# Kernel tuning notes

Hardware: AMD Instinct MI355X
Metric: run time of the kernel (lower is better)

The kernel has to match this reference:

```python
import jax, jax.numpy as jnp
import numpy as np

B, S, H = 4096, 15, 1024
PQ, CFG = 1003, 128
IN = PQ + 5 + 10 + 3 + 3  # 1024, matches input_size in torch module
EPS = 1e-5


def lstm_cell(x, h, c, Wih, Whh, bih, bhh):
    # PyTorch LSTMCell gate order: i, f, g, o
    gates = x @ Wih.T + bih + h @ Whh.T + bhh
    i, f, g, o = jnp.split(gates, 4, axis=-1)
    c2 = jax.nn.sigmoid(f) * c + jax.nn.sigmoid(i) * jnp.tanh(g)
    h2 = jax.nn.sigmoid(o) * jnp.tanh(c2)
    return h2, c2


def setup_inputs() -> dict:
    key = jax.random.key(0)
    ks = jax.random.split(key, 16)
    g = lambda i, shape, s=0.02: jax.random.normal(ks[i], shape, jnp.float32) * s
    u = lambda i, shape: jax.random.uniform(ks[i], shape, jnp.float32, -1.0, 1.0)
    return {
        "input_p_q": jax.random.normal(ks[0], (B, S, PQ), jnp.float32),
        "input_config": jax.random.normal(ks[1], (B, S, CFG), jnp.float32),
        "input_time": jax.random.randint(ks[2], (B, S, 3), 0, 5),
        "W_cfg": g(3, (10, CFG)), "b_cfg": jnp.zeros((10,), jnp.float32),
        "emb_hour": g(4, (24, 5), 1.0),
        "emb_weekday": g(5, (8, 3), 1.0),
        "emb_season": g(6, (5, 3), 1.0),
        # init(): uniform(-1,1) weights, zero bias for the two attention layers
        "W_sa": u(7, (IN, IN + 2 * H)), "b_sa": jnp.zeros((IN,), jnp.float32),
        "Wih_s": g(8, (4 * H, IN)), "Whh_s": g(9, (4 * H, H)),
        "bih_s": jnp.zeros((4 * H,), jnp.float32), "bhh_s": jnp.zeros((4 * H,), jnp.float32),
        "Wih_t": g(10, (4 * H, H)), "Whh_t": g(11, (4 * H, H)),
        "bih_t": jnp.zeros((4 * H,), jnp.float32), "bhh_t": jnp.zeros((4 * H,), jnp.float32),
        "W_ta": u(12, (1, 3 * H)), "b_ta": jnp.zeros((1,), jnp.float32),
        "bn_gamma": jnp.ones((S,), jnp.float32), "bn_beta": jnp.zeros((S,), jnp.float32),
        "Wih_d": g(13, (4, H)), "Whh_d": g(14, (4, 1)),
        "bih_d": jnp.zeros((4,), jnp.float32), "bhh_d": jnp.zeros((4,), jnp.float32),
    }


def reference(input_p_q, input_config, input_time,
              W_cfg, b_cfg, emb_hour, emb_weekday, emb_season,
              W_sa, b_sa, Wih_s, Whh_s, bih_s, bhh_s,
              Wih_t, Whh_t, bih_t, bhh_t, W_ta, b_ta,
              bn_gamma, bn_beta, Wih_d, Whh_d, bih_d, bhh_d):
    cfg = input_config @ W_cfg.T + b_cfg                       # [B,S,10]
    hr = emb_hour[input_time[:, :, 0]]                         # [B,S,5]
    wd = emb_weekday[input_time[:, :, 1]]                      # [B,S,3]
    sn = emb_season[input_time[:, :, 2]]                       # [B,S,3]
    inputs = jnp.concatenate([input_p_q, cfg, hr, wd, sn], axis=2)  # [B,S,IN]

    Bsz, Ssz = inputs.shape[0], inputs.shape[1]
    Hd = Whh_s.shape[1]
    h0 = jnp.zeros((Bsz, Hd), inputs.dtype)

    # ---- spatial encoder with per-step attention gating ----
    def step1(carry, x):
        h, c = carry
        score = jnp.tanh(jnp.concatenate([h, c, x], axis=1) @ W_sa.T + b_sa)
        h2, c2 = lstm_cell(x * score, h, c, Wih_s, Whh_s, bih_s, bhh_s)
        return (h2, c2), h2

    _, mid = jax.lax.scan(step1, (h0, h0), jnp.swapaxes(inputs, 0, 1))  # [S,B,H]
    mid = jnp.swapaxes(mid, 0, 1)                                      # [B,S,H]

    # ---- BatchNorm1d(15) in training mode: channels = sequence dim ----
    mu = mid.mean(axis=(0, 2), keepdims=True)
    var = mid.var(axis=(0, 2), keepdims=True)  # biased variance, as torch uses for normalization
    mid = (mid - mu) * jax.lax.rsqrt(var + EPS) * bn_gamma[None, :, None] + bn_beta[None, :, None]

    # ---- temporal encoder with post-step attention score ----
    def step2(carry, x):
        h, c = carry
        h2, c2 = lstm_cell(x, h, c, Wih_t, Whh_t, bih_t, bhh_t)
        att = jnp.tanh(jnp.concatenate([h2, c2, x], axis=1) @ W_ta.T + b_ta)  # [B,1]
        return (h2, c2), (h2, att)

    _, (outs, att2) = jax.lax.scan(step2, (h0, h0), jnp.swapaxes(mid, 0, 1))
    outs = jnp.swapaxes(outs, 0, 1)   # [B,S,H]
    att2 = jnp.swapaxes(att2, 0, 1)   # [B,S,1]

    # ---- decoder nn.LSTM (batch_first=False!) scans over the BATCH axis ----
    hd0 = jnp.zeros((Ssz, 1), outs.dtype)

    def step3(carry, x):
        h, c = carry
        h2, c2 = lstm_cell(x, h, c, Wih_d, Whh_d, bih_d, bhh_d)
        return (h2, c2), h2

    _, out1d = jax.lax.scan(step3, (hd0, hd0), outs)  # [B,S,1]

    sm = jax.nn.softmax(att2, axis=1)  # [B,S,1]
    # bmm(out1d^T [B,1,S], sm [B,S,1]) -> [B,1,1]
    out = jnp.einsum('bs,bs->b', out1d[:, :, 0], sm[:, :, 0])[:, None, None]
    return out
```

## Files before the change

kernel.cpp:

```cpp
#include <hip/hip_runtime.h>

#define AS1 __attribute__((address_space(1)))
#define AS3 __attribute__((address_space(3)))

typedef __attribute__((ext_vector_type(8))) _Float16 f16x8;
typedef __attribute__((ext_vector_type(4))) float f32x4;

static constexpr int BATCH = 4096;
static constexpr int SEQ   = 15;

__device__ __forceinline__ float h2f(unsigned short u) {
  return (float)__builtin_bit_cast(_Float16, u);
}
__device__ __forceinline__ unsigned short f2h(float f) {
  return __builtin_bit_cast(unsigned short, (_Float16)f);
}
__device__ __forceinline__ float frcp(float x) { return __builtin_amdgcn_rcpf(x); }
__device__ __forceinline__ float sigm(float x)  { return frcp(1.0f + __expf(-x)); }
__device__ __forceinline__ float tanhx(float x) { return 1.0f - 2.0f * frcp(1.0f + __expf(2.0f * x)); }

template<int STAGE>
__global__ __launch_bounds__(512, 2)
void gemm_lstm256(const unsigned short* A0, int lda0, int K0,
                  const unsigned short* A1, int lda1,
                  const unsigned short* Bw, int K,
                  const float* ib, float* Cst,
                  unsigned short* P0, unsigned short* P1, unsigned short* P2,
                  float* F0)
{
  __shared__ unsigned short lds[2][2][16384];
  const int tid  = threadIdx.x;
  const int wid  = tid >> 6;
  const int lane = tid & 63;
  const int wr = wid >> 2;
  const int wc = wid & 3;
  const int NT = K >> 6;

  const int bid = blockIdx.y * gridDim.x + blockIdx.x;
  const int cpx = (gridDim.x * gridDim.y) >> 3;
  const int swz = (bid & 7) * cpx + (bid >> 3);
  const int row0 = (swz / gridDim.x) * 256;
  const int col0 = (swz % gridDim.x) * 256;

  auto stage_half = [&](int bb, int mat, int hh, int kt) {
    const int k0 = kt * 64;
    const unsigned short* Ap; int lda, kc, rb;
    if (mat == 0) {
      if (k0 < K0) { Ap = A0; lda = lda0; kc = k0; }
      else         { Ap = A1; lda = lda1; kc = k0 - K0; }
      rb = row0;
    } else { Ap = Bw; lda = K; kc = k0; rb = col0; }
#pragma unroll
    for (int i = 0; i < 2; ++i) {
      const int x  = (tid + i * 512) * 16;
      const int xs = x ^ (((x >> 9) & 1) << 5);
      const int r  = hh * 128 + (xs >> 7);
      const int cb = xs & 127;
      const unsigned short* src = Ap + (size_t)(rb + r) * lda + kc + (cb >> 1);
      __builtin_amdgcn_global_load_lds((const AS1 void*)src,
          (AS3 void*)((char*)&lds[bb][mat][0] + hh * 16384 + wid * 1024 + i * 8192),
          16, 0, 0);
    }
  };

  const int frow = lane & 15;
  const int axor = ((lane >> 2) & 1) << 5;
  const int abase = ((((wr * 128 + frow) << 7) + (((lane >> 4) & 3) << 4))) ^ axor;
  const int bbase = ((((wc * 64  + frow) << 7) + (((lane >> 4) & 3) << 4))) ^ axor;

  const f32x4 zero = {0.f, 0.f, 0.f, 0.f};
  f32x4 acc[8][4];
#pragma unroll
  for (int i = 0; i < 8; ++i)
#pragma unroll
    for (int j = 0; j < 4; ++j) acc[i][j] = zero;

  stage_half(0, 0, 0, 0);
  stage_half(0, 0, 1, 0);
  stage_half(0, 1, 0, 0);
  stage_half(0, 1, 1, 0);
  if (NT > 1) { stage_half(1, 1, 0, 1); stage_half(1, 1, 1, 1); }
  asm volatile("s_waitcnt vmcnt(4)" ::: "memory");
  __builtin_amdgcn_s_barrier();

#define DO_PHASE(MB, STG, VMW)                                                        \
  {                                                                                   \
    const f16x8 a0 = *(const f16x8*)(ldsA + abase + (MB)     * 2048);                 \
    const f16x8 a1 = *(const f16x8*)(ldsA + abase + (MB)     * 2048 + 64);            \
    const f16x8 a2 = *(const f16x8*)(ldsA + abase + (MB + 1) * 2048);                 \
    const f16x8 a3 = *(const f16x8*)(ldsA + abase + (MB + 1) * 2048 + 64);            \
    STG;                                                                              \
    __builtin_amdgcn_s_barrier();                                                     \
    asm volatile("s_waitcnt lgkmcnt(0)" ::: "memory");                                \
    __builtin_amdgcn_sched_barrier(0);                                                \
    __builtin_amdgcn_s_setprio(1);                                                    \
    _Pragma("unroll")                                                                 \
    for (int n = 0; n < 4; ++n) {                                                     \
      acc[MB][n]     = __builtin_amdgcn_mfma_f32_16x16x32_f16(a0, bv[n][0], acc[MB][n],     0, 0, 0); \
      acc[MB][n]     = __builtin_amdgcn_mfma_f32_16x16x32_f16(a1, bv[n][1], acc[MB][n],     0, 0, 0); \
      acc[MB + 1][n] = __builtin_amdgcn_mfma_f32_16x16x32_f16(a2, bv[n][0], acc[MB + 1][n], 0, 0, 0); \
      acc[MB + 1][n] = __builtin_amdgcn_mfma_f32_16x16x32_f16(a3, bv[n][1], acc[MB + 1][n], 0, 0, 0); \
    }                                                                                 \
    __builtin_amdgcn_s_setprio(0);                                                    \
    VMW;                                                                              \
    __builtin_amdgcn_s_barrier();                                                     \
  }

  for (int kt = 0; kt < NT; ++kt) {
    const int cur = kt & 1;
    const char* ldsA = (const char*)&lds[cur][0][0];
    const char* ldsB = (const char*)&lds[cur][1][0];
    f16x8 bv[4][2];
#pragma unroll
    for (int n = 0; n < 4; ++n) {
      bv[n][0] = *(const f16x8*)(ldsB + bbase + n * 2048);
      bv[n][1] = *(const f16x8*)(ldsB + bbase + n * 2048 + 64);
    }
    DO_PHASE(0, { if (kt + 1 < NT) stage_half(cur ^ 1, 0, 0, kt + 1); }, { (void)0; });
    DO_PHASE(2, { if (kt + 1 < NT) stage_half(cur ^ 1, 0, 1, kt + 1); }, { (void)0; });
    DO_PHASE(4, { if (kt + 2 < NT) stage_half(cur,     1, 0, kt + 2); }, { (void)0; });
    DO_PHASE(6, { if (kt + 2 < NT) stage_half(cur,     1, 1, kt + 2); },
             { if (kt >= NT - 2) { asm volatile("s_waitcnt vmcnt(0)" ::: "memory"); }
               else              { asm volatile("s_waitcnt vmcnt(4)" ::: "memory"); } });
  }
#undef DO_PHASE

  float* xw = ((float*)&lds[0][0][0]) + wid * 256;
  const int cs = lane & 3;
  const int er = (lane >> 4) << 2;
  const int uq = (lane >> 2) & 3;

  float cold[8][4];
#pragma unroll
  for (int mi = 0; mi < 8; ++mi)
#pragma unroll
    for (int ni = 0; ni < 4; ++ni) {
      const int R = row0 + wr * 128 + mi * 16 + er + cs;
      const int U = ((col0 + wc * 64 + ni * 16) >> 2) + uq;
      cold[mi][ni] = Cst[(size_t)R * 1024 + U];
    }

#pragma unroll
  for (int mi = 0; mi < 8; ++mi)
#pragma unroll
    for (int ni = 0; ni < 4; ++ni) {
      __builtin_amdgcn_wave_barrier();
      *(f32x4*)(xw + lane * 4) = acc[mi][ni];
      __builtin_amdgcn_wave_barrier();
      __builtin_amdgcn_sched_barrier(0);
      const int qb = (lane & 60) * 4;
      const float g0 = xw[qb + 0  + cs];
      const float g1 = xw[qb + 4  + cs];
      const float g2 = xw[qb + 8  + cs];
      const float g3 = xw[qb + 12 + cs];
      __builtin_amdgcn_wave_barrier();
      const int R = row0 + wr * 128 + mi * 16 + er + cs;
      const int U = ((col0 + wc * 64 + ni * 16) >> 2) + uq;
      const f32x4 b4 = *(const f32x4*)(ib + 4 * U);
      const float gi = g0 + b4[0];
      const float gf = g1 + b4[1];
      const float gg = g2 + b4[2];
      const float go = g3 + b4[3];
      const size_t off = (size_t)R * 1024 + U;
      const float cn = sigm(gf) * cold[mi][ni] + sigm(gi) * tanhx(gg);
      const float hn = sigm(go) * tanhx(cn);
      Cst[off] = cn;
      const unsigned short hb = f2h(hn);
      if (STAGE == 1) {
        P0[(size_t)R * 2048 + U]        = hb;
        P0[(size_t)R * 2048 + 1024 + U] = f2h(cn);
        P1[(size_t)R * 2048 + 1024 + U] = hb;
        P2[off] = hb;
      } else {
        F0[off] = hn;
        P0[off] = hb;
      }
    }
}

template<int BM, int BN, int NWM, int NWN>
__global__ __launch_bounds__(256)
void gemm_score(const unsigned short* A0, int lda0, int K0,
                const unsigned short* A1, int lda1,
                const unsigned short* Bw,
                const float* bias, const unsigned short* X,
                unsigned short* OutG, int ldo, int N, int K)
{
  static_assert(NWM * NWN == 4, "4 waves");
  constexpr int FM = BM / (NWM * 16);
  constexpr int FN = BN / (NWN * 16);
  __shared__ unsigned short As[BM * 64];
  __shared__ unsigned short Bs[BN * 64];
  const int tid  = threadIdx.x;
  const int wid  = tid >> 6;
  const int lane = tid & 63;
  const int bid = blockIdx.y * gridDim.x + blockIdx.x;
  const int cpx = (gridDim.x * gridDim.y) >> 3;
  const int swz = (bid & 7) * cpx + (bid >> 3);
  const int row0 = (swz / gridDim.x) * BM;
  const int col0 = (swz % gridDim.x) * BN;
  const int wr = wid / NWN;
  const int wc = wid % NWN;
  const int l8 = lane >> 3;
  const int l7 = (lane & 7) * 8;
  const int frow = lane & 15;
  const int fcol = (lane >> 4) * 8;

  const f32x4 zero = {0.f, 0.f, 0.f, 0.f};
  f32x4 acc[FM][FN];
#pragma unroll
  for (int i = 0; i < FM; ++i)
#pragma unroll
    for (int j = 0; j < FN; ++j) acc[i][j] = zero;

  for (int k0 = 0; k0 < K; k0 += 64) {
    __syncthreads();
    const unsigned short* Ap; int lda, kc;
    if (k0 < K0) { Ap = A0; lda = lda0; kc = k0; }
    else         { Ap = A1; lda = lda1; kc = k0 - K0; }
#pragma unroll
    for (int ch = 0; ch < BM / 32; ++ch) {
      const int c = ch * 4 + wid;
      const unsigned short* src = Ap + (size_t)(row0 + c * 8 + l8) * lda + kc + l7;
      __builtin_amdgcn_global_load_lds((const AS1 void*)src, (AS3 void*)(As + c * 512), 16, 0, 0);
    }
#pragma unroll
    for (int ch = 0; ch < BN / 32; ++ch) {
      const int c = ch * 4 + wid;
      const unsigned short* src = Bw + (size_t)(col0 + c * 8 + l8) * K + k0 + l7;
      __builtin_amdgcn_global_load_lds((const AS1 void*)src, (AS3 void*)(Bs + c * 512), 16, 0, 0);
    }
    __syncthreads();
#pragma unroll
    for (int kk = 0; kk < 2; ++kk) {
      f16x8 av[FM], bv[FN];
#pragma unroll
      for (int mi = 0; mi < FM; ++mi)
        av[mi] = *(const f16x8*)(As + (wr * FM * 16 + mi * 16 + frow) * 64 + kk * 32 + fcol);
#pragma unroll
      for (int ni = 0; ni < FN; ++ni)
        bv[ni] = *(const f16x8*)(Bs + (wc * FN * 16 + ni * 16 + frow) * 64 + kk * 32 + fcol);
#pragma unroll
      for (int mi = 0; mi < FM; ++mi)
#pragma unroll
        for (int ni = 0; ni < FN; ++ni)
          acc[mi][ni] = __builtin_amdgcn_mfma_f32_16x16x32_f16(av[mi], bv[ni], acc[mi][ni], 0, 0, 0);
    }
  }

  const int erow = (lane >> 4) * 4;
#pragma unroll
  for (int mi = 0; mi < FM; ++mi)
#pragma unroll
    for (int ni = 0; ni < FN; ++ni) {
      const int row = row0 + wr * FM * 16 + mi * 16 + erow;
      const int col = col0 + wc * FN * 16 + ni * 16 + frow;
      const float bs = bias[col];
#pragma unroll
      for (int r = 0; r < 4; ++r) {
        const float v = tanhx(acc[mi][ni][r] + bs);
        const float xv = h2f(X[(size_t)(row + r) * N + col]);
        OutG[(size_t)(row + r) * ldo + col] = f2h(xv * v);
      }
    }
}

__global__ void f2h_copy(const float* src, unsigned short* dst, int n) {
  const int i = blockIdx.x * 256 + threadIdx.x;
  if (i < n) dst[i] = f2h(src[i]);
}

__global__ void cat_w_int(const float* wih, const float* whh, unsigned short* dst) {
  const int i = blockIdx.x * 256 + threadIdx.x;
  const int n = i >> 11, k = i & 2047;
  const int u = n >> 2, g = n & 3;
  const int src = g * 1024 + u;
  dst[i] = f2h(k < 1024 ? wih[src * 1024 + k] : whh[src * 1024 + (k - 1024)]);
}

__global__ void prep_bias(const float* bih, const float* bhh, float* ib) {
  const int i = blockIdx.x * 256 + threadIdx.x;
  const int u = i >> 2, g = i & 3;
  ib[i] = bih[g * 1024 + u] + bhh[g * 1024 + u];
}

__global__ void copy_pq(const float* pq, unsigned short* inb) {
  const int i4 = blockIdx.x * 256 + threadIdx.x;
  const float4 v = ((const float4*)pq)[i4];
  const int base = i4 * 4;
  const float vv[4] = {v.x, v.y, v.z, v.w};
#pragma unroll
  for (int e = 0; e < 4; ++e) {
    const int idx = base + e;
    const int bt = idx / 1003;
    const int j = idx - bt * 1003;
    const int b = bt / 15;
    const int t = bt - b * 15;
    inb[((size_t)t * BATCH + b) * 1024 + j] = f2h(vv[e]);
  }
}

__global__ void cfg_emb(const float* cfg, const int* tim,
                        const float* Wc, const float* bc,
                        const float* eh, const float* ew, const float* es,
                        unsigned short* inb)
{
  const int wv = (blockIdx.x * 256 + threadIdx.x) >> 6;
  const int lane = threadIdx.x & 63;
  const int b = wv / 15, t = wv - b * 15;
  const float* cp = cfg + (size_t)wv * 128;
  const float c0 = cp[lane], c1v = cp[lane + 64];
  unsigned short* dst = inb + ((size_t)t * BATCH + b) * 1024;
#pragma unroll
  for (int g = 0; g < 10; ++g) {
    float v = fmaf(c0, Wc[g * 128 + lane], c1v * Wc[g * 128 + 64 + lane]);
    v += __shfl_xor(v, 32); v += __shfl_xor(v, 16); v += __shfl_xor(v, 8);
    v += __shfl_xor(v, 4);  v += __shfl_xor(v, 2);  v += __shfl_xor(v, 1);
    if (lane == 0) dst[1003 + g] = f2h(v + bc[g]);
  }
  if (lane < 5)       dst[1013 + lane] = f2h(eh[tim[wv * 3 + 0] * 5 + lane]);
  else if (lane < 8)  dst[1018 + (lane - 5)] = f2h(ew[tim[wv * 3 + 1] * 3 + (lane - 5)]);
  else if (lane < 11) dst[1021 + (lane - 8)] = f2h(es[tim[wv * 3 + 2] * 3 + (lane - 8)]);
}

__global__ void bn_partial(const unsigned short* mid, float* part) {
  const int t = blockIdx.y, blk = blockIdx.x, tid = threadIdx.x;
  const unsigned short* p = mid + (size_t)t * BATCH * 1024;
  float s = 0.f, ss = 0.f;
  for (int i = blk * 256 + tid; i < BATCH * 1024; i += 128 * 256) {
    const float v = h2f(p[i]);
    s += v; ss += v * v;
  }
  for (int o = 32; o > 0; o >>= 1) { s += __shfl_down(s, o); ss += __shfl_down(ss, o); }
  __shared__ float sm[8];
  if ((tid & 63) == 0) { sm[(tid >> 6) * 2] = s; sm[(tid >> 6) * 2 + 1] = ss; }
  __syncthreads();
  if (tid == 0) {
    part[(t * 128 + blk) * 2]     = sm[0] + sm[2] + sm[4] + sm[6];
    part[(t * 128 + blk) * 2 + 1] = sm[1] + sm[3] + sm[5] + sm[7];
  }
}

__global__ void bn_final(const float* part, const float* gamma, const float* beta, float* scsh) {
  const int t = blockIdx.x, tid = threadIdx.x;
  float s = part[(t * 128 + tid) * 2], ss = part[(t * 128 + tid) * 2 + 1];
  for (int o = 32; o > 0; o >>= 1) { s += __shfl_down(s, o); ss += __shfl_down(ss, o); }
  __shared__ float sm[4];
  if ((tid & 63) == 0) { sm[(tid >> 6) * 2] = s; sm[(tid >> 6) * 2 + 1] = ss; }
  __syncthreads();
  if (tid == 0) {
    const float S = sm[0] + sm[2], SS = sm[1] + sm[3];
    const float inv = 1.f / (float)(BATCH * 1024);
    const float mu = S * inv;
    const float var = SS * inv - mu * mu;
    const float rstd = rsqrtf(var + 1e-5f);
    const float sc = rstd * gamma[t];
    scsh[t * 2] = sc;
    scsh[t * 2 + 1] = beta[t] - mu * sc;
  }
}

__global__ void bn_apply(unsigned short* mid, const float* scsh) {
  const int t = blockIdx.y;
  const int i = blockIdx.x * 256 + threadIdx.x;
  unsigned short* p = mid + (size_t)t * BATCH * 1024;
  p[i] = f2h(h2f(p[i]) * scsh[t * 2] + scsh[t * 2 + 1]);
}

__global__ void att_proj(const float* h2, const float* c2, const unsigned short* xn,
                         const float* Wta, const float* bta, const float* Wihd,
                         float* att2, float* proj, int t)
{
  const int b = blockIdx.x, tid = threadIdx.x;
  const float* h = h2 + (size_t)b * 1024;
  const float* c = c2 + (size_t)b * 1024;
  const unsigned short* x = xn + (size_t)b * 1024;
  float a = 0.f, p0 = 0.f, p1 = 0.f, p2 = 0.f, p3 = 0.f;
  for (int j = tid; j < 1024; j += 256) {
    const float hv = h[j], cv = c[j], xv = h2f(x[j]);
    a  += hv * Wta[j] + cv * Wta[1024 + j] + xv * Wta[2048 + j];
    p0 += hv * Wihd[j];
    p1 += hv * Wihd[1024 + j];
    p2 += hv * Wihd[2048 + j];
    p3 += hv * Wihd[3072 + j];
  }
  for (int o = 32; o > 0; o >>= 1) {
    a  += __shfl_down(a, o);  p0 += __shfl_down(p0, o); p1 += __shfl_down(p1, o);
    p2 += __shfl_down(p2, o); p3 += __shfl_down(p3, o);
  }
  __shared__ float sm[4][5];
  if ((tid & 63) == 0) {
    const int w = tid >> 6;
    sm[w][0] = a; sm[w][1] = p0; sm[w][2] = p1; sm[w][3] = p2; sm[w][4] = p3;
  }
  __syncthreads();
  if (tid == 0) {
    att2[b * SEQ + t] = tanhx(sm[0][0] + sm[1][0] + sm[2][0] + sm[3][0] + bta[0]);
    float* pp = proj + ((size_t)b * SEQ + t) * 4;
    pp[0] = sm[0][1] + sm[1][1] + sm[2][1] + sm[3][1];
    pp[1] = sm[0][2] + sm[1][2] + sm[2][2] + sm[3][2];
    pp[2] = sm[0][3] + sm[1][3] + sm[2][3] + sm[3][3];
    pp[3] = sm[0][4] + sm[1][4] + sm[2][4] + sm[3][4];
  }
}

__global__ __launch_bounds__(256) void lstm3_par(
    const float* proj, const float* Whhd,
    const float* bihd, const float* bhhd, float* out1d)
{
  const int s = blockIdx.x;
  const int tid = threadIdx.x;
  constexpr int CH = BATCH / 256;
  const float wi = Whhd[0], wf = Whhd[1], wg = Whhd[2], wo = Whhd[3];
  const float bi = bihd[0] + bhhd[0], bf_ = bihd[1] + bhhd[1];
  const float bg = bihd[2] + bhhd[2], bo = bihd[3] + bhhd[3];
  const float4* p4 = (const float4*)proj;
  float4 p[CH];
#pragma unroll
  for (int u = 0; u < CH; ++u) p[u] = p4[(tid * CH + u) * SEQ + s];
  __shared__ float Hb[257], Cb[257];
  Hb[tid] = 0.f; Cb[tid] = 0.f;
  if (tid == 255) { Hb[256] = 0.f; Cb[256] = 0.f; }
  __syncthreads();
  float h, c;
  for (int it = 0; it < 8; ++it) {
    h = Hb[tid]; c = Cb[tid];
#pragma unroll
    for (int u = 0; u < CH; ++u) {
      const float gi = fmaf(h, wi, p[u].x + bi);
      const float gf = fmaf(h, wf, p[u].y + bf_);
      const float gg = fmaf(h, wg, p[u].z + bg);
      const float go = fmaf(h, wo, p[u].w + bo);
      c = sigm(gf) * c + sigm(gi) * tanhx(gg);
      h = sigm(go) * tanhx(c);
    }
    __syncthreads();
    Hb[tid + 1] = h; Cb[tid + 1] = c;
    __syncthreads();
  }
  h = Hb[tid]; c = Cb[tid];
#pragma unroll
  for (int u = 0; u < CH; ++u) {
    const float gi = fmaf(h, wi, p[u].x + bi);
    const float gf = fmaf(h, wf, p[u].y + bf_);
    const float gg = fmaf(h, wg, p[u].z + bg);
    const float go = fmaf(h, wo, p[u].w + bo);
    c = sigm(gf) * c + sigm(gi) * tanhx(gg);
    h = sigm(go) * tanhx(c);
    out1d[(tid * CH + u) * SEQ + s] = h;
  }
}

__global__ void finalize_k(const float* att2, const float* out1d, float* out) {
  const int b = blockIdx.x * 64 + threadIdx.x;
  const float* a = att2 + b * SEQ;
  const float* o = out1d + b * SEQ;
  float m = -1e30f;
  for (int s = 0; s < SEQ; ++s) m = fmaxf(m, a[s]);
  float den = 0.f, num = 0.f;
  for (int s = 0; s < SEQ; ++s) {
    const float e = __expf(a[s] - m);
    den += e; num += e * o[s];
  }
  out[b] = num / den;
}

extern "C" void kernel_launch(void* const* d_in, const int* in_sizes, int n_in,
                              void* d_out, int out_size, void* d_ws, size_t ws_size,
                              hipStream_t stream)
{
  (void)in_sizes; (void)n_in; (void)out_size; (void)ws_size;
  const float* in_pq   = (const float*)d_in[0];
  const float* in_cfg  = (const float*)d_in[1];
  const int*   in_time = (const int*)d_in[2];
  const float* W_cfg   = (const float*)d_in[3];
  const float* b_cfg   = (const float*)d_in[4];
  const float* emb_h   = (const float*)d_in[5];
  const float* emb_w   = (const float*)d_in[6];
  const float* emb_s   = (const float*)d_in[7];
  const float* W_sa    = (const float*)d_in[8];
  const float* b_sa    = (const float*)d_in[9];
  const float* Wih_s   = (const float*)d_in[10];
  const float* Whh_s   = (const float*)d_in[11];
  const float* bih_s   = (const float*)d_in[12];
  const float* bhh_s   = (const float*)d_in[13];
  const float* Wih_t   = (const float*)d_in[14];
  const float* Whh_t   = (const float*)d_in[15];
  const float* bih_t   = (const float*)d_in[16];
  const float* bhh_t   = (const float*)d_in[17];
  const float* W_ta    = (const float*)d_in[18];
  const float* b_ta    = (const float*)d_in[19];
  const float* gamma   = (const float*)d_in[20];
  const float* beta    = (const float*)d_in[21];
  const float* Wih_d   = (const float*)d_in[22];
  const float* Whh_d   = (const float*)d_in[23];
  const float* bih_d   = (const float*)d_in[24];
  const float* bhh_d   = (const float*)d_in[25];
  float* out = (float*)d_out;

  char* w = (char*)d_ws;
  size_t off = 0;
  auto alloc = [&](size_t bytes) -> char* {
    char* p = w + off;
    off = (off + bytes + 255) & ~(size_t)255;
    return p;
  };
  unsigned short* inb  = (unsigned short*)alloc((size_t)SEQ * BATCH * 1024 * 2);
  unsigned short* hc   = (unsigned short*)alloc((size_t)BATCH * 2048 * 2);
  unsigned short* gA0  = (unsigned short*)alloc((size_t)BATCH * 2048 * 2);
  unsigned short* gA1  = (unsigned short*)alloc((size_t)BATCH * 2048 * 2);
  float*          c1   = (float*)alloc((size_t)BATCH * 1024 * 4);
  unsigned short* h2b0 = (unsigned short*)alloc((size_t)BATCH * 1024 * 2);
  unsigned short* h2b1 = (unsigned short*)alloc((size_t)BATCH * 1024 * 2);
  float*          h2f_ = (float*)alloc((size_t)BATCH * 1024 * 4);
  float*          c2f  = (float*)alloc((size_t)BATCH * 1024 * 4);
  unsigned short* wsab = (unsigned short*)alloc((size_t)1024 * 3072 * 2);
  unsigned short* w1   = (unsigned short*)alloc((size_t)4096 * 2048 * 2);
  unsigned short* w2   = (unsigned short*)alloc((size_t)4096 * 2048 * 2);
  float*          ib1  = (float*)alloc(4096 * 4);
  float*          ib2  = (float*)alloc(4096 * 4);
  float*          part = (float*)alloc(15 * 128 * 2 * 4);
  float*          scsh = (float*)alloc(15 * 2 * 4);
  float*          att2 = (float*)alloc((size_t)BATCH * SEQ * 4);
  float*          proj = (float*)alloc((size_t)BATCH * SEQ * 4 * 4);
  float*          o1d  = (float*)alloc((size_t)BATCH * SEQ * 4);

  unsigned short* gAbuf[2]  = {gA0, gA1};
  unsigned short* h2bbuf[2] = {h2b0, h2b1};

  hipMemsetAsync(hc,   0, (size_t)BATCH * 2048 * 2, stream);
  hipMemsetAsync(gA0,  0, (size_t)BATCH * 2048 * 2, stream);
  hipMemsetAsync(c1,   0, (size_t)BATCH * 1024 * 4, stream);
  hipMemsetAsync(h2b0, 0, (size_t)BATCH * 1024 * 2, stream);
  hipMemsetAsync(c2f,  0, (size_t)BATCH * 1024 * 4, stream);

  f2h_copy<<<(1024 * 3072) / 256, 256, 0, stream>>>(W_sa, wsab, 1024 * 3072);
  cat_w_int<<<(4096 * 2048) / 256, 256, 0, stream>>>(Wih_s, Whh_s, w1);
  cat_w_int<<<(4096 * 2048) / 256, 256, 0, stream>>>(Wih_t, Whh_t, w2);
  prep_bias<<<16, 256, 0, stream>>>(bih_s, bhh_s, ib1);
  prep_bias<<<16, 256, 0, stream>>>(bih_t, bhh_t, ib2);
  copy_pq<<<(BATCH * SEQ * 1003 / 4) / 256, 256, 0, stream>>>(in_pq, inb);
  cfg_emb<<<(BATCH * SEQ) / 4, 256, 0, stream>>>(in_cfg, in_time, W_cfg, b_cfg,
                                                 emb_h, emb_w, emb_s, inb);

  for (int t = 0; t < SEQ; ++t) {
    unsigned short* xt = inb + (size_t)t * BATCH * 1024;
    gemm_score<128, 64, 4, 1><<<dim3(1024 / 64, BATCH / 128), 256, 0, stream>>>(
        hc, 2048, 2048, xt, 1024, wsab, b_sa, xt, gAbuf[t & 1], 2048, 1024, 3072);
    gemm_lstm256<1><<<dim3(4096 / 256, BATCH / 256), 512, 0, stream>>>(
        gAbuf[t & 1], 2048, 2048, gAbuf[t & 1], 2048, w1, 2048,
        ib1, c1, hc, gAbuf[(t + 1) & 1], xt, nullptr);
  }

  bn_partial<<<dim3(128, SEQ), 256, 0, stream>>>(inb, part);
  bn_final<<<SEQ, 128, 0, stream>>>(part, gamma, beta, scsh);
  bn_apply<<<dim3((BATCH * 1024) / 256, SEQ), 256, 0, stream>>>(inb, scsh);

  for (int t = 0; t < SEQ; ++t) {
    const unsigned short* xt = inb + (size_t)t * BATCH * 1024;
    gemm_lstm256<2><<<dim3(4096 / 256, BATCH / 256), 512, 0, stream>>>(
        xt, 1024, 1024, h2bbuf[t & 1], 1024, w2, 2048,
        ib2, c2f, h2bbuf[(t + 1) & 1], nullptr, nullptr, h2f_);
    att_proj<<<BATCH, 256, 0, stream>>>(h2f_, c2f, xt, W_ta, b_ta, Wih_d, att2, proj, t);
  }

  lstm3_par<<<SEQ, 256, 0, stream>>>(proj, Whh_d, bih_d, bhh_d, o1d);
  finalize_k<<<BATCH / 64, 64, 0, stream>>>(att2, o1d, out);
}
```

Baseline: 4.003 ms.

## Rewrite attention score GEMM as 256x128 tile double-buffered pipelined kernel

```diff
diff --git a/kernel.cpp b/kernel.cpp
--- a/kernel.cpp
+++ b/kernel.cpp
@@ -178,89 +178,131 @@
     }
 }
 
-template<int BM, int BN, int NWM, int NWN>
-__global__ __launch_bounds__(256)
-void gemm_score(const unsigned short* A0, int lda0, int K0,
-                const unsigned short* A1, int lda1,
-                const unsigned short* Bw,
-                const float* bias, const unsigned short* X,
-                unsigned short* OutG, int ldo, int N, int K)
+__global__ __launch_bounds__(512, 2)
+void gemm_score256(const unsigned short* A0, int lda0, int K0,
+                   const unsigned short* A1, int lda1,
+                   const unsigned short* Bw, int K,
+                   const float* bias, const unsigned short* X,
+                   unsigned short* OutG)
 {
-  static_assert(NWM * NWN == 4, "4 waves");
-  constexpr int FM = BM / (NWM * 16);
-  constexpr int FN = BN / (NWN * 16);
-  __shared__ unsigned short As[BM * 64];
-  __shared__ unsigned short Bs[BN * 64];
+  __shared__ unsigned short lds[2][24576];
   const int tid  = threadIdx.x;
   const int wid  = tid >> 6;
   const int lane = tid & 63;
+  const int wr = wid >> 2;
+  const int wc = wid & 3;
+  const int NT = K >> 6;
+
   const int bid = blockIdx.y * gridDim.x + blockIdx.x;
   const int cpx = (gridDim.x * gridDim.y) >> 3;
   const int swz = (bid & 7) * cpx + (bid >> 3);
-  const int row0 = (swz / gridDim.x) * BM;
-  const int col0 = (swz % gridDim.x) * BN;
-  const int wr = wid / NWN;
-  const int wc = wid % NWN;
-  const int l8 = lane >> 3;
-  const int l7 = (lane & 7) * 8;
+  const int row0 = (swz / gridDim.x) * 256;
+  const int col0 = (swz % gridDim.x) * 128;
+
+  auto stage_half = [&](int bb, int mat, int hh, int kt) {
+    const int k0 = kt * 64;
+    if (mat == 0) {
+      const unsigned short* Ap; int lda, kc;
+      if (k0 < K0) { Ap = A0; lda = lda0; kc = k0; }
+      else         { Ap = A1; lda = lda1; kc = k0 - K0; }
+#pragma unroll
+      for (int i = 0; i < 2; ++i) {
+        const int x  = (tid + i * 512) * 16;
+        const int xs = x ^ (((x >> 9) & 1) << 5);
+        const int r  = hh * 128 + (xs >> 7);
+        const int cb = xs & 127;
+        const unsigned short* src = Ap + (size_t)(row0 + r) * lda + kc + (cb >> 1);
+        __builtin_amdgcn_global_load_lds((const AS1 void*)src,
+            (AS3 void*)((char*)&lds[bb][0] + hh * 16384 + wid * 1024 + i * 8192),
+            16, 0, 0);
+      }
+    } else {
+      const int x  = tid * 16;
+      const int xs = x ^ (((x >> 9) & 1) << 5);
+      const int r  = hh * 64 + (xs >> 7);
+      const int cb = xs & 127;
+      const unsigned short* src = Bw + (size_t)(col0 + r) * K + k0 + (cb >> 1);
+      __builtin_amdgcn_global_load_lds((const AS1 void*)src,
+          (AS3 void*)((char*)&lds[bb][0] + 32768 + hh * 8192 + wid * 1024),
+          16, 0, 0);
+    }
+  };
+
   const int frow = lane & 15;
-  const int fcol = (lane >> 4) * 8;
+  const int axor = ((lane >> 2) & 1) << 5;
+  const int abase = ((((wr * 128 + frow) << 7) + (((lane >> 4) & 3) << 4))) ^ axor;
+  const int bbase = ((((wc * 32  + frow) << 7) + (((lane >> 4) & 3) << 4))) ^ axor;
 
   const f32x4 zero = {0.f, 0.f, 0.f, 0.f};
-  f32x4 acc[FM][FN];
-#pragma unroll
-  for (int i = 0; i < FM; ++i)
-#pragma unroll
-    for (int j = 0; j < FN; ++j) acc[i][j] = zero;
-
-  for (int k0 = 0; k0 < K; k0 += 64) {
-    __syncthreads();
-    const unsigned short* Ap; int lda, kc;
-    if (k0 < K0) { Ap = A0; lda = lda0; kc = k0; }
-    else         { Ap = A1; lda = lda1; kc = k0 - K0; }
-#pragma unroll
-    for (int ch = 0; ch < BM / 32; ++ch) {
-      const int c = ch * 4 + wid;
-      const unsigned short* src = Ap + (size_t)(row0 + c * 8 + l8) * lda + kc + l7;
-      __builtin_amdgcn_global_load_lds((const AS1 void*)src, (AS3 void*)(As + c * 512), 16, 0, 0);
-    }
-#pragma unroll
-    for (int ch = 0; ch < BN / 32; ++ch) {
-      const int c = ch * 4 + wid;
-      const unsigned short* src = Bw + (size_t)(col0 + c * 8 + l8) * K + k0 + l7;
-      __builtin_amdgcn_global_load_lds((const AS1 void*)src, (AS3 void*)(Bs + c * 512), 16, 0, 0);
-    }
-    __syncthreads();
-#pragma unroll
-    for (int kk = 0; kk < 2; ++kk) {
-      f16x8 av[FM], bv[FN];
-#pragma unroll
-      for (int mi = 0; mi < FM; ++mi)
-        av[mi] = *(const f16x8*)(As + (wr * FM * 16 + mi * 16 + frow) * 64 + kk * 32 + fcol);
-#pragma unroll
-      for (int ni = 0; ni < FN; ++ni)
-        bv[ni] = *(const f16x8*)(Bs + (wc * FN * 16 + ni * 16 + frow) * 64 + kk * 32 + fcol);
-#pragma unroll
-      for (int mi = 0; mi < FM; ++mi)
-#pragma unroll
-        for (int ni = 0; ni < FN; ++ni)
-          acc[mi][ni] = __builtin_amdgcn_mfma_f32_16x16x32_f16(av[mi], bv[ni], acc[mi][ni], 0, 0, 0);
-    }
-  }
-
-  const int erow = (lane >> 4) * 4;
-#pragma unroll
-  for (int mi = 0; mi < FM; ++mi)
-#pragma unroll
-    for (int ni = 0; ni < FN; ++ni) {
-      const int row = row0 + wr * FM * 16 + mi * 16 + erow;
-      const int col = col0 + wc * FN * 16 + ni * 16 + frow;
+  f32x4 acc[8][2];
+#pragma unroll
+  for (int i = 0; i < 8; ++i)
+#pragma unroll
+    for (int j = 0; j < 2; ++j) acc[i][j] = zero;
+
+  stage_half(0, 0, 0, 0);
+  stage_half(0, 0, 1, 0);
+  stage_half(0, 1, 0, 0);
+  stage_half(0, 1, 1, 0);
+  if (NT > 1) { stage_half(1, 1, 0, 1); stage_half(1, 1, 1, 1); }
+  asm volatile("s_waitcnt vmcnt(2)" ::: "memory");
+  __builtin_amdgcn_s_barrier();
+
+#define DO_PHASE_S(MB, STG, VMW)                                                      \
+  {                                                                                   \
+    const f16x8 a0 = *(const f16x8*)(ldsA + abase + (MB)     * 2048);                 \
+    const f16x8 a1 = *(const f16x8*)(ldsA + abase + (MB)     * 2048 + 64);            \
+    const f16x8 a2 = *(const f16x8*)(ldsA + abase + (MB + 1) * 2048);                 \
+    const f16x8 a3 = *(const f16x8*)(ldsA + abase + (MB + 1) * 2048 + 64);            \
+    STG;                                                                              \
+    __builtin_amdgcn_s_barrier();                                                     \
+    asm volatile("s_waitcnt lgkmcnt(0)" ::: "memory");                                \
+    __builtin_amdgcn_sched_barrier(0);                                                \
+    __builtin_amdgcn_s_setprio(1);                                                    \
+    _Pragma("unroll")                                                                 \
+    for (int n = 0; n < 2; ++n) {                                                     \
+      acc[MB][n]     = __builtin_amdgcn_mfma_f32_16x16x32_f16(a0, bv[n][0], acc[MB][n],     0, 0, 0); \
+      acc[MB][n]     = __builtin_amdgcn_mfma_f32_16x16x32_f16(a1, bv[n][1], acc[MB][n],     0, 0, 0); \
+      acc[MB + 1][n] = __builtin_amdgcn_mfma_f32_16x16x32_f16(a2, bv[n][0], acc[MB + 1][n], 0, 0, 0); \
+      acc[MB + 1][n] = __builtin_amdgcn_mfma_f32_16x16x32_f16(a3, bv[n][1], acc[MB + 1][n], 0, 0, 0); \
+    }                                                                                 \
+    __builtin_amdgcn_s_setprio(0);                                                    \
+    VMW;                                                                              \
+    __builtin_amdgcn_s_barrier();                                                     \
+  }
+
+  for (int kt = 0; kt < NT; ++kt) {
+    const int cur = kt & 1;
+    const char* ldsA = (const char*)&lds[cur][0];
+    const char* ldsB = ldsA + 32768;
+    f16x8 bv[2][2];
+#pragma unroll
+    for (int n = 0; n < 2; ++n) {
+      bv[n][0] = *(const f16x8*)(ldsB + bbase + n * 2048);
+      bv[n][1] = *(const f16x8*)(ldsB + bbase + n * 2048 + 64);
+    }
+    DO_PHASE_S(0, { if (kt + 1 < NT) stage_half(cur ^ 1, 0, 0, kt + 1); }, { (void)0; });
+    DO_PHASE_S(2, { if (kt + 1 < NT) stage_half(cur ^ 1, 0, 1, kt + 1); }, { (void)0; });
+    DO_PHASE_S(4, { if (kt + 2 < NT) stage_half(cur,     1, 0, kt + 2); }, { (void)0; });
+    DO_PHASE_S(6, { if (kt + 2 < NT) stage_half(cur,     1, 1, kt + 2); },
+             { if (kt >= NT - 2) { asm volatile("s_waitcnt vmcnt(0)" ::: "memory"); }
+               else              { asm volatile("s_waitcnt vmcnt(2)" ::: "memory"); } });
+  }
+#undef DO_PHASE_S
+
+  const int er = (lane >> 4) << 2;
+#pragma unroll
+  for (int mi = 0; mi < 8; ++mi)
+#pragma unroll
+    for (int ni = 0; ni < 2; ++ni) {
+      const int row = row0 + wr * 128 + mi * 16 + er;
+      const int col = col0 + wc * 32 + ni * 16 + frow;
       const float bs = bias[col];
 #pragma unroll
       for (int r = 0; r < 4; ++r) {
         const float v = tanhx(acc[mi][ni][r] + bs);
-        const float xv = h2f(X[(size_t)(row + r) * N + col]);
-        OutG[(size_t)(row + r) * ldo + col] = f2h(xv * v);
+        const float xv = h2f(X[(size_t)(row + r) * 1024 + col]);
+        OutG[(size_t)(row + r) * 2048 + col] = f2h(xv * v);
       }
     }
 }
@@ -545,8 +587,8 @@
 
   for (int t = 0; t < SEQ; ++t) {
     unsigned short* xt = inb + (size_t)t * BATCH * 1024;
-    gemm_score<128, 64, 4, 1><<<dim3(1024 / 64, BATCH / 128), 256, 0, stream>>>(
-        hc, 2048, 2048, xt, 1024, wsab, b_sa, xt, gAbuf[t & 1], 2048, 1024, 3072);
+    gemm_score256<<<dim3(1024 / 128, BATCH / 256), 512, 0, stream>>>(
+        hc, 2048, 2048, xt, 1024, wsab, 3072, b_sa, xt, gAbuf[t & 1]);
     gemm_lstm256<1><<<dim3(4096 / 256, BATCH / 256), 512, 0, stream>>>(
         gAbuf[t & 1], 2048, 2048, gAbuf[t & 1], 2048, w1, 2048,
         ib1, c1, hc, gAbuf[(t + 1) & 1], xt, nullptr);
```

After: 4.206 ms. 5.1% more time.
